# Optimization experiments

Hardware: AMD Instinct MI355X
Metric: run time of the kernel (lower is better)

Reference implementation:

```python
import jax, jax.numpy as jnp
import numpy as np

B, T, C, H = 8, 1024, 768, 12
HD = C // H  # 64, even for RoPE
ROPE_THETA = 10000.0


def precompute_freqs_cis(dim, end, theta=ROPE_THETA):
    # [end, dim//2, 2] with (cos, sin) in last axis
    freqs = 1.0 / theta ** (jnp.arange(0, dim // 2).astype(jnp.float32) / (dim // 2))
    t = jnp.arange(end)
    f = jnp.outer(t, freqs)
    return jnp.stack([jnp.cos(f), jnp.sin(f)], axis=-1)


def apply_rope(x, fc):
    # x: [B,T,H,hd]; fc: [T,1,hd//2,2] (broadcasts over B and H)
    xr = x.reshape(*x.shape[:-1], -1, 2)
    x_re, x_im = xr[..., 0], xr[..., 1]
    cos, sin = fc[..., 0], fc[..., 1]
    out_re = x_re * cos - x_im * sin
    out_im = x_re * sin + x_im * cos
    return jnp.stack([out_re, out_im], axis=-1).reshape(x.shape)


def setup_inputs() -> dict:
    key = jax.random.key(0)
    k0, k1, k2 = jax.random.split(key, 3)
    x = jax.random.normal(k0, (B, T, C), jnp.float32)
    Wqkv = jax.random.normal(k1, (C, 3 * C), jnp.float32) * 0.02
    bqkv = jnp.zeros((3 * C,), jnp.float32)
    Wproj = jax.random.normal(k2, (C, C), jnp.float32) * 0.02
    bproj = jnp.zeros((C,), jnp.float32)
    mask = jnp.tril(jnp.ones((T, T), jnp.int32))  # causal
    return {"x": x, "Wqkv": Wqkv, "bqkv": bqkv, "Wproj": Wproj, "bproj": bproj, "mask": mask}


def reference(x, Wqkv, bqkv, Wproj, bproj, mask):
    B_, T_, C_ = x.shape
    qkv = (x @ Wqkv + bqkv).reshape(B_, T_, 3, H, HD)
    q, k, v = qkv[:, :, 0], qkv[:, :, 1], qkv[:, :, 2]  # each [B,T,H,hd]
    fc = precompute_freqs_cis(HD, T_)[:, None]  # [T,1,hd//2,2]
    q = apply_rope(q, fc)
    k = apply_rope(k, fc)
    scale = 1.0 / jnp.sqrt(jnp.float32(HD))
    attn = jnp.einsum('bthd,bkhd->bhtk', q, k) * scale  # [B,H,T,T]
    neg = jnp.finfo(attn.dtype).min
    attn = jnp.where(mask[None, None, :, :] == 0, neg, attn)
    attn = jax.nn.softmax(attn, axis=-1)
    out = jnp.einsum('bhtk,bkhd->bthd', attn, v).reshape(B_, T_, C_)
    return out @ Wproj + bproj
```

## Files before the change

kernel.cpp:

```cpp
#include <hip/hip_runtime.h>
#include <cstdint>
#include <cstddef>

#define BB 8
#define TT 1024
#define CC 768
#define NH 12
#define HD 64

using bf16x8 = __attribute__((ext_vector_type(8))) short;
using f32x4  = __attribute__((ext_vector_type(4))) float;

static __device__ __forceinline__ short f2bf(float f) {
    uint32_t u;
    __builtin_memcpy(&u, &f, 4);
    u += 0x7FFFu + ((u >> 16) & 1u);
    return (short)(u >> 16);
}

static __device__ __forceinline__ uint32_t bfpack(float lo, float hi) {
    return (uint32_t)(uint16_t)f2bf(lo) | ((uint32_t)(uint16_t)f2bf(hi) << 16);
}

#define GLOAD_LDS16(gp, lp)                                                        \
    __builtin_amdgcn_global_load_lds(                                              \
        (const __attribute__((address_space(1))) void*)(gp),                       \
        (__attribute__((address_space(3))) void*)(lp), 16, 0, 0)

__global__ void fc_kernel(float2* __restrict__ fc) {
    int idx = blockIdx.x * 256 + threadIdx.x;
    int t = idx >> 5, p = idx & 31;
    float freq = powf(10000.0f, -(float)p / 32.0f);
    float a = (float)t * freq;
    fc[idx] = make_float2(cosf(a), sinf(a));
}

__global__ __launch_bounds__(256)
void cast_kernel(const float* __restrict__ in, short* __restrict__ out) {
    int i = (blockIdx.x * 256 + threadIdx.x) * 8;
    float4 f0 = *(const float4*)(in + i);
    float4 f1 = *(const float4*)(in + i + 4);
    bf16x8 h;
    h[0] = f2bf(f0.x); h[1] = f2bf(f0.y); h[2] = f2bf(f0.z); h[3] = f2bf(f0.w);
    h[4] = f2bf(f1.x); h[5] = f2bf(f1.y); h[6] = f2bf(f1.z); h[7] = f2bf(f1.w);
    *(bf16x8*)(out + i) = h;
}

__global__ __launch_bounds__(256)
void transpose_cast_kernel(const float* __restrict__ in, short* __restrict__ out,
                           int R, int Cdim) {
    __shared__ float tile[32][33];
    int tx = threadIdx.x, ty = threadIdx.y;
    int c0 = blockIdx.x * 32, r0 = blockIdx.y * 32;
#pragma unroll
    for (int i = 0; i < 4; i++)
        tile[ty + 8 * i][tx] = in[(size_t)(r0 + ty + 8 * i) * Cdim + c0 + tx];
    __syncthreads();
#pragma unroll
    for (int i = 0; i < 4; i++)
        out[(size_t)(c0 + ty + 8 * i) * R + r0 + tx] = f2bf(tile[tx][ty + 8 * i]);
}

__global__ __launch_bounds__(256)
void vtrans_kernel(const short* __restrict__ V, short* __restrict__ VT) {
    __shared__ short tl[64][72];
    const int tid = threadIdx.x;
    const int bh = blockIdx.y, t0 = blockIdx.x * 64;
    {
        int r = tid >> 2, cs = (tid & 3) * 16;
        const short* src = V + (size_t)bh * TT * HD + (size_t)(t0 + r) * HD + cs;
        *(bf16x8*)&tl[r][cs]     = *(const bf16x8*)src;
        *(bf16x8*)&tl[r][cs + 8] = *(const bf16x8*)(src + 8);
    }
    __syncthreads();
    {
        int d = tid >> 2, ts = (tid & 3) * 16;
        bf16x8 o0, o1;
#pragma unroll
        for (int e = 0; e < 8; e++) { o0[e] = tl[ts + e][d]; o1[e] = tl[ts + 8 + e][d]; }
        short* dst = VT + (size_t)bh * TT * HD + (size_t)d * TT + t0 + ts;
        *(bf16x8*)dst       = o0;
        *(bf16x8*)(dst + 8) = o1;
    }
}

template <int EPI>
__global__ __launch_bounds__(512, 2)
void gemm_kernel(const short* __restrict__ Agl, const short* __restrict__ BT,
                 const float* __restrict__ bias,
                 short* __restrict__ Qb, short* __restrict__ Kb, short* __restrict__ Vb,
                 const float2* __restrict__ fc, float* __restrict__ out) {
    __shared__ __align__(16) char smem[131072];
    const int tid = threadIdx.x;
    const int lane = tid & 63, wid = tid >> 6;
    const int g = lane >> 4, c = lane & 15;
    const int wm = wid >> 2, wn = wid & 3;

    const int nx = gridDim.x;
    const int bid = blockIdx.y * nx + blockIdx.x;
    const int cpx = (nx * gridDim.y) >> 3;
    const int swz = (bid & 7) * cpx + (bid >> 3);
    const int m0 = (swz / nx) * 256, n0 = (swz % nx) * 256;

    const int srow = (lane >> 2);
    const int schunk = (lane & 3) ^ ((lane >> 3) & 3);
    const short* Ab0 = Agl + (size_t)(m0 + wid * 16 + srow) * 768 + schunk * 8;
    const short* Bb0 = BT  + (size_t)(n0 + wid * 16 + srow) * 768 + schunk * 8;

#define STAGE(S, T)                                                              \
    {                                                                            \
        size_t ko = (size_t)(T) * 32;                                            \
        GLOAD_LDS16(Ab0 + ko,             smem + (S) * 32768 + wid * 1024);      \
        GLOAD_LDS16(Ab0 + 128 * 768 + ko, smem + (S) * 32768 + 8192 + wid * 1024); \
        GLOAD_LDS16(Bb0 + ko,             smem + (S) * 32768 + 16384 + wid * 1024); \
        GLOAD_LDS16(Bb0 + 128 * 768 + ko, smem + (S) * 32768 + 24576 + wid * 1024); \
    }

    const f32x4 zero4 = {0.f, 0.f, 0.f, 0.f};
    f32x4 acc[8][4];
#pragma unroll
    for (int i = 0; i < 8; i++)
#pragma unroll
        for (int j = 0; j < 4; j++) acc[i][j] = zero4;

    const int rchunk16 = (g ^ ((c >> 1) & 3)) << 4;

    STAGE(0, 0);
    STAGE(1, 1);
    STAGE(2, 2);
    asm volatile("s_waitcnt vmcnt(8)" ::: "memory");
    asm volatile("s_barrier" ::: "memory");

    for (int w4 = 0; w4 < 24; w4 += 4) {
#pragma unroll
        for (int ww = 0; ww < 4; ww++) {
            const int W = w4 + ww;
            int tileS = W + 3;
            if (tileS >= 24) tileS -= 24;
            const char* slot = smem + ww * 32768;

            bf16x8 af[8], bfr[4];
#pragma unroll
            for (int mi = 0; mi < 8; mi++) {
                af[mi] = *(const bf16x8*)(slot + wm * 8192 + (mi * 16 + c) * 64 + rchunk16);
            }
#pragma unroll
            for (int ni = 0; ni < 4; ni++) {
                bfr[ni] = *(const bf16x8*)(slot + 16384 + (wn >> 1) * 8192 +
                                           ((wn & 1) * 64 + ni * 16 + c) * 64 + rchunk16);
            }
            STAGE((W + 3) & 3, tileS);
            __builtin_amdgcn_s_setprio(1);
#pragma unroll
            for (int mi = 0; mi < 8; mi++)
#pragma unroll
                for (int ni = 0; ni < 4; ni++)
                    acc[mi][ni] = __builtin_amdgcn_mfma_f32_16x16x32_bf16(
                        af[mi], bfr[ni], acc[mi][ni], 0, 0, 0);
            __builtin_amdgcn_s_setprio(0);
            asm volatile("s_waitcnt vmcnt(8)" ::: "memory");
            asm volatile("s_barrier" ::: "memory");
        }
    }

    asm volatile("s_waitcnt vmcnt(0)" ::: "memory");
    asm volatile("s_barrier" ::: "memory");

    if (EPI == 0) {
        uint32_t* LD = (uint32_t*)smem;
#pragma unroll
        for (int ni = 0; ni < 4; ni++) {
            int nl = wn * 64 + ni * 16 + c;
            int n = n0 + nl;
            float bv = bias[n];
            int part = (n >= 1536) ? 2 : (n >= 768 ? 1 : 0);
            int d = (n - part * 768) & 63;
#pragma unroll
            for (int mi = 0; mi < 8; mi++) {
#pragma unroll
                for (int r = 0; r < 4; r++) {
                    int ml = wm * 128 + mi * 16 + g * 4 + r;
                    float v = acc[mi][ni][r] + bv;
                    float pv = __shfl_xor(v, 1);
                    if (!(c & 1)) {
                        float o0, o1;
                        if (part < 2) {
                            int t = (m0 + ml) & 1023;
                            float2 cs = fc[t * 32 + (d >> 1)];
                            o0 = v * cs.x - pv * cs.y;
                            o1 = v * cs.y + pv * cs.x;
                            if (part == 0) { o0 *= 0.125f; o1 *= 0.125f; }
                        } else { o0 = v; o1 = pv; }
                        LD[ml * 128 + ((nl >> 1) ^ ((ml & 7) << 2))] = bfpack(o0, o1);
                    }
                }
            }
        }
        __syncthreads();
#pragma unroll
        for (int p = 0; p < 8; p++) {
            int ml = p * 32 + (tid >> 4);
            int sw = (ml & 7) << 2;
            int wc = (tid & 15) * 8;
            int4 d0 = *(const int4*)&LD[ml * 128 + (wc ^ sw)];
            int4 d1 = *(const int4*)&LD[ml * 128 + ((wc + 4) ^ sw)];
            int n = n0 + wc * 2;
            int part = (n >= 1536) ? 2 : (n >= 768 ? 1 : 0);
            int rem = n - part * 768;
            int h = rem >> 6, d = rem & 63;
            int m = m0 + ml, b = m >> 10, t = m & 1023;
            short* dst = (part == 0 ? Qb : part == 1 ? Kb : Vb)
                         + (((size_t)b * NH + h) * TT + t) * HD + d;
            *(int4*)dst = d0;
            *(int4*)(dst + 8) = d1;
        }
    } else {
#pragma unroll
        for (int mi = 0; mi < 8; mi++)
#pragma unroll
            for (int ni = 0; ni < 4; ni++) {
                int n = n0 + wn * 64 + ni * 16 + c;
                float bv = bias[n];
#pragma unroll
                for (int r = 0; r < 4; r++) {
                    int m = m0 + wm * 128 + mi * 16 + g * 4 + r;
                    out[(size_t)m * CC + n] = acc[mi][ni][r] + bv;
                }
            }
    }
#undef STAGE
}

__global__ __launch_bounds__(256)
void attn_kernel(const short* __restrict__ Qb, const short* __restrict__ Kb,
                 const short* __restrict__ VT, short* __restrict__ Ob) {
    __shared__ uint32_t Pt[4][32][32];
    __shared__ uint32_t ot[128 * 32];
    const int tid = threadIdx.x, lane = tid & 63, wid = tid >> 6;
    const int g = lane >> 4, c = lane & 15;
    const int bh = blockIdx.x, qb = 7 - (int)blockIdx.y;
    const int b = bh / NH, h = bh % NH;
    const short* Qp = Qb + (size_t)bh * TT * HD;
    const short* Kp = Kb + (size_t)bh * TT * HD;
    const short* Vp = VT + (size_t)bh * TT * HD;
    const int q0 = qb * 128 + wid * 32;
    const int sw = (c & 7) << 2;

    bf16x8 qf[2][2];
#pragma unroll
    for (int qs = 0; qs < 2; qs++)
#pragma unroll
        for (int kh = 0; kh < 2; kh++)
            qf[qs][kh] = *(const bf16x8*)(Qp + (size_t)(q0 + qs * 16 + c) * HD + kh * 32 + g * 8);

    const f32x4 zero4 = {0.f, 0.f, 0.f, 0.f};
    f32x4 o[2][4];
#pragma unroll
    for (int qs = 0; qs < 2; qs++)
#pragma unroll
        for (int dt = 0; dt < 4; dt++) o[qs][dt] = zero4;
    float mrun[2] = {-1e30f, -1e30f}, lrun[2] = {0.f, 0.f};

    const int t0max = ((q0 + 31) >> 6) << 6;
    for (int t0 = 0; t0 <= t0max; t0 += 64) {
        f32x4 st[2][4];
#pragma unroll
        for (int nt = 0; nt < 4; nt++) {
            const short* kp = Kp + (size_t)(t0 + nt * 16 + c) * HD + g * 8;
            bf16x8 k0 = *(const bf16x8*)kp;
            bf16x8 k1 = *(const bf16x8*)(kp + 32);
#pragma unroll
            for (int qs = 0; qs < 2; qs++) {
                f32x4 z = zero4;
                z = __builtin_amdgcn_mfma_f32_16x16x32_bf16(k0, qf[qs][0], z, 0, 0, 0);
                z = __builtin_amdgcn_mfma_f32_16x16x32_bf16(k1, qf[qs][1], z, 0, 0, 0);
                st[qs][nt] = z;
            }
        }
        bf16x8 vf[2][4];
#pragma unroll
        for (int blk = 0; blk < 2; blk++)
#pragma unroll
            for (int dt = 0; dt < 4; dt++)
                vf[blk][dt] = *(const bf16x8*)(Vp + (size_t)(dt * 16 + c) * TT + t0 + blk * 32 + g * 8);
        if (t0 + 63 > q0) {
#pragma unroll
            for (int qs = 0; qs < 2; qs++) {
                int q = q0 + qs * 16 + c;
#pragma unroll
                for (int nt = 0; nt < 4; nt++)
#pragma unroll
                    for (int r = 0; r < 4; r++)
                        if (t0 + nt * 16 + g * 4 + r > q) st[qs][nt][r] = -1e30f;
            }
        }
#pragma unroll
        for (int qs = 0; qs < 2; qs++) {
            float mx = st[qs][0][0];
#pragma unroll
            for (int nt = 0; nt < 4; nt++)
#pragma unroll
                for (int r = 0; r < 4; r++) mx = fmaxf(mx, st[qs][nt][r]);
            mx = fmaxf(mx, __shfl_xor(mx, 16));
            mx = fmaxf(mx, __shfl_xor(mx, 32));
            float mnew = fmaxf(mrun[qs], mx);
            float al = __expf(mrun[qs] - mnew);
            mrun[qs] = mnew;
            float sm = 0.f;
#pragma unroll
            for (int nt = 0; nt < 4; nt++)
#pragma unroll
                for (int r = 0; r < 4; r++) {
                    float e = __expf(st[qs][nt][r] - mnew);
                    st[qs][nt][r] = e;
                    sm += e;
                }
            sm += __shfl_xor(sm, 16);
            sm += __shfl_xor(sm, 32);
            lrun[qs] = lrun[qs] * al + sm;
#pragma unroll
            for (int dt = 0; dt < 4; dt++) {
                o[qs][dt][0] *= al; o[qs][dt][1] *= al;
                o[qs][dt][2] *= al; o[qs][dt][3] *= al;
            }
            int row = qs * 16 + c;
#pragma unroll
            for (int nt = 0; nt < 4; nt++) {
                uint32_t w0 = bfpack(st[qs][nt][0], st[qs][nt][1]);
                uint32_t w1 = bfpack(st[qs][nt][2], st[qs][nt][3]);
                int wa = nt * 8 + 2 * g;
                Pt[wid][row][wa ^ sw]       = w0;
                Pt[wid][row][(wa + 1) ^ sw] = w1;
            }
        }
#pragma unroll
        for (int qs = 0; qs < 2; qs++) {
            int row = qs * 16 + c;
#pragma unroll
            for (int blk = 0; blk < 2; blk++) {
                bf16x8 pf = *(const bf16x8*)&Pt[wid][row][(blk * 16 + 4 * g) ^ sw];
#pragma unroll
                for (int dt = 0; dt < 4; dt++)
                    o[qs][dt] = __builtin_amdgcn_mfma_f32_16x16x32_bf16(
                        vf[blk][dt], pf, o[qs][dt], 0, 0, 0);
            }
        }
    }

#pragma unroll
    for (int qs = 0; qs < 2; qs++) {
        float inv = 1.0f / lrun[qs];
        int ql = wid * 32 + qs * 16 + c;
#pragma unroll
        for (int dt = 0; dt < 4; dt++) {
            uint32_t w0 = bfpack(o[qs][dt][0] * inv, o[qs][dt][1] * inv);
            uint32_t w1 = bfpack(o[qs][dt][2] * inv, o[qs][dt][3] * inv);
            int jc0 = dt * 8 + 2 * g;
            int jc1 = jc0 + 1;
            ot[ql * 32 + ((((jc0 >> 2) ^ (c & 7)) << 2) | (jc0 & 3))] = w0;
            ot[ql * 32 + ((((jc1 >> 2) ^ (c & 7)) << 2) | (jc1 & 3))] = w1;
        }
    }
    __syncthreads();
#pragma unroll
    for (int p = 0; p < 4; p++) {
        int q = (tid >> 3) + 32 * p;
        int jb = tid & 7;
        const uint32_t* src = &ot[q * 32 + ((jb ^ (q & 7)) << 2)];
        int4 w = *(const int4*)src;
        *(int4*)(Ob + ((size_t)b * TT + qb * 128 + q) * CC + h * HD + jb * 8) = w;
    }
}

extern "C" void kernel_launch(void* const* d_in, const int* in_sizes, int n_in,
                              void* d_out, int out_size, void* d_ws, size_t ws_size,
                              hipStream_t stream) {
    const float* x     = (const float*)d_in[0];
    const float* Wqkv  = (const float*)d_in[1];
    const float* bqkv  = (const float*)d_in[2];
    const float* Wproj = (const float*)d_in[3];
    const float* bproj = (const float*)d_in[4];

    char* ws = (char*)d_ws;
    short*  WqkvT  = (short*)(ws);
    short*  WprojT = (short*)(ws + 3538944);
    float2* fc     = (float2*)(ws + 3538944 + 1179648);
    short*  Qb     = (short*)(ws + 4980736);
    short*  Kb     = (short*)(ws + 4980736 + 1 * 12582912);
    short*  VOb    = (short*)(ws + 4980736 + 2 * 12582912);
    short*  VbT    = (short*)(ws + 4980736 + 3 * 12582912);
    short*  xb     = VbT;
    float*  out    = (float*)d_out;

    hipLaunchKernelGGL(fc_kernel, dim3(128), dim3(256), 0, stream, fc);
    hipLaunchKernelGGL(transpose_cast_kernel, dim3(72, 24), dim3(32, 8), 0, stream,
                       Wqkv, WqkvT, 768, 2304);
    hipLaunchKernelGGL(transpose_cast_kernel, dim3(24, 24), dim3(32, 8), 0, stream,
                       Wproj, WprojT, 768, 768);
    hipLaunchKernelGGL(cast_kernel, dim3(3072), dim3(256), 0, stream, x, xb);
    hipLaunchKernelGGL((gemm_kernel<0>), dim3(9, 32), dim3(512), 0, stream,
                       xb, WqkvT, bqkv, Qb, Kb, VOb, fc, (float*)nullptr);
    hipLaunchKernelGGL(vtrans_kernel, dim3(16, 96), dim3(256), 0, stream, VOb, VbT);
    hipLaunchKernelGGL(attn_kernel, dim3(96, 8), dim3(256), 0, stream, Qb, Kb, VbT, VOb);
    hipLaunchKernelGGL((gemm_kernel<1>), dim3(3, 32), dim3(512), 0, stream,
                       VOb, WprojT, bproj,
                       (short*)nullptr, (short*)nullptr, (short*)nullptr,
                       (const float2*)nullptr, out);
}
```

Before: 193.3 us.

## Split GEMM k-step into two half-phases interleaving A/B staging with MFMA

The QKV and projection GEMM main loop is split into two phases per k-tile. The A-tile prefetch is issued before the first half of the MFMAs and the B-tile prefetch before the second half, each followed by a barrier. Only four A fragments are held at a time, which lowers register pressure. The LDS XOR swizzle is also changed to key on the row's low two bits rather than bits 1–2. The aim is finer overlap of global-to-LDS loads with matrix math, at the cost of two extra workgroup barriers per k-step.

```diff
diff --git a/kernel.cpp b/kernel.cpp
--- a/kernel.cpp
+++ b/kernel.cpp
@@ -102,18 +102,19 @@
     const int swz = (bid & 7) * cpx + (bid >> 3);
     const int m0 = (swz / nx) * 256, n0 = (swz % nx) * 256;
 
-    const int srow = (lane >> 2);
-    const int schunk = (lane & 3) ^ ((lane >> 3) & 3);
-    const short* Ab0 = Agl + (size_t)(m0 + wid * 16 + srow) * 768 + schunk * 8;
-    const short* Bb0 = BT  + (size_t)(n0 + wid * 16 + srow) * 768 + schunk * 8;
-
-#define STAGE(S, T)                                                              \
+    const int sc = (((tid & 3) ^ ((tid >> 2) & 3)) << 3);
+    const short* Ab0 = Agl + (size_t)(m0 + (tid >> 2)) * 768 + sc;
+    const short* Bb0 = BT  + (size_t)(n0 + (tid >> 2)) * 768 + sc;
+
+#define STAGE_A(S, T)                                                            \
     {                                                                            \
-        size_t ko = (size_t)(T) * 32;                                            \
-        GLOAD_LDS16(Ab0 + ko,             smem + (S) * 32768 + wid * 1024);      \
-        GLOAD_LDS16(Ab0 + 128 * 768 + ko, smem + (S) * 32768 + 8192 + wid * 1024); \
-        GLOAD_LDS16(Bb0 + ko,             smem + (S) * 32768 + 16384 + wid * 1024); \
-        GLOAD_LDS16(Bb0 + 128 * 768 + ko, smem + (S) * 32768 + 24576 + wid * 1024); \
+        GLOAD_LDS16(Ab0 + (size_t)(T) * 32,             smem + (S) * 32768 + wid * 1024); \
+        GLOAD_LDS16(Ab0 + (size_t)128 * 768 + (T) * 32, smem + (S) * 32768 + 8192 + wid * 1024); \
+    }
+#define STAGE_B(S, T)                                                            \
+    {                                                                            \
+        GLOAD_LDS16(Bb0 + (size_t)(T) * 32,             smem + (S) * 32768 + 16384 + wid * 1024); \
+        GLOAD_LDS16(Bb0 + (size_t)128 * 768 + (T) * 32, smem + (S) * 32768 + 24576 + wid * 1024); \
     }
 
     const f32x4 zero4 = {0.f, 0.f, 0.f, 0.f};
@@ -123,40 +124,56 @@
 #pragma unroll
         for (int j = 0; j < 4; j++) acc[i][j] = zero4;
 
-    const int rchunk16 = (g ^ ((c >> 1) & 3)) << 4;
-
-    STAGE(0, 0);
-    STAGE(1, 1);
-    STAGE(2, 2);
+    const int rk = ((g ^ (c & 3)) << 4);
+
+    STAGE_A(0, 0); STAGE_B(0, 0);
+    STAGE_A(1, 1); STAGE_B(1, 1);
+    STAGE_A(2, 2); STAGE_B(2, 2);
     asm volatile("s_waitcnt vmcnt(8)" ::: "memory");
     asm volatile("s_barrier" ::: "memory");
 
-    for (int w4 = 0; w4 < 24; w4 += 4) {
-#pragma unroll
-        for (int ww = 0; ww < 4; ww++) {
-            const int W = w4 + ww;
-            int tileS = W + 3;
-            if (tileS >= 24) tileS -= 24;
-            const char* slot = smem + ww * 32768;
-
-            bf16x8 af[8], bfr[4];
-#pragma unroll
-            for (int mi = 0; mi < 8; mi++) {
-                af[mi] = *(const bf16x8*)(slot + wm * 8192 + (mi * 16 + c) * 64 + rchunk16);
-            }
-#pragma unroll
-            for (int ni = 0; ni < 4; ni++) {
-                bfr[ni] = *(const bf16x8*)(slot + 16384 + (wn >> 1) * 8192 +
-                                           ((wn & 1) * 64 + ni * 16 + c) * 64 + rchunk16);
-            }
-            STAGE((W + 3) & 3, tileS);
+    for (int t4 = 0; t4 < 24; t4 += 4) {
+#pragma unroll
+        for (int tt = 0; tt < 4; tt++) {
+            const int T = t4 + tt;
+            const int slotR = tt;
+            const int slotS = (tt + 3) & 3;
+            int Ts = T + 3;
+            if (Ts >= 24) Ts -= 24;
+            const char* sA = smem + slotR * 32768;
+            const char* sB = sA + 16384;
+
+            bf16x8 bfr[4], af[4];
+#pragma unroll
+            for (int ni = 0; ni < 4; ni++)
+                bfr[ni] = *(const bf16x8*)(sB + (wn * 64 + ni * 16 + c) * 64 + rk);
+#pragma unroll
+            for (int mi = 0; mi < 4; mi++)
+                af[mi] = *(const bf16x8*)(sA + (wm * 128 + mi * 16 + c) * 64 + rk);
+            STAGE_A(slotS, Ts);
+            asm volatile("s_barrier" ::: "memory");
             __builtin_amdgcn_s_setprio(1);
 #pragma unroll
-            for (int mi = 0; mi < 8; mi++)
+            for (int mi = 0; mi < 4; mi++)
 #pragma unroll
                 for (int ni = 0; ni < 4; ni++)
                     acc[mi][ni] = __builtin_amdgcn_mfma_f32_16x16x32_bf16(
                         af[mi], bfr[ni], acc[mi][ni], 0, 0, 0);
+            __builtin_amdgcn_s_setprio(0);
+            asm volatile("s_barrier" ::: "memory");
+
+#pragma unroll
+            for (int mi = 0; mi < 4; mi++)
+                af[mi] = *(const bf16x8*)(sA + (wm * 128 + (4 + mi) * 16 + c) * 64 + rk);
+            STAGE_B(slotS, Ts);
+            asm volatile("s_barrier" ::: "memory");
+            __builtin_amdgcn_s_setprio(1);
+#pragma unroll
+            for (int mi = 0; mi < 4; mi++)
+#pragma unroll
+                for (int ni = 0; ni < 4; ni++)
+                    acc[4 + mi][ni] = __builtin_amdgcn_mfma_f32_16x16x32_bf16(
+                        af[mi], bfr[ni], acc[4 + mi][ni], 0, 0, 0);
             __builtin_amdgcn_s_setprio(0);
             asm volatile("s_waitcnt vmcnt(8)" ::: "memory");
             asm volatile("s_barrier" ::: "memory");
@@ -228,7 +245,8 @@
                 }
             }
     }
-#undef STAGE
+#undef STAGE_A
+#undef STAGE_B
 }
 
 __global__ __launch_bounds__(256)
```

Measured after the change: 202.8 us. 4.9% more time.
